# Kernel optimization log

Hardware: AMD Instinct MI355X
Metric: run time of the kernel (lower is better)

The kernel has to match this reference:

```python
import jax, jax.numpy as jnp
import numpy as np

HEAD_DIM = 64
NUM_FEATURES = 256


def _sample_orf(head_dim, num_features, seed=0):
    """Orthogonal random features with chi(d)-norm row scaling (FAVOR+)."""
    rng = np.random.RandomState(seed)
    blocks = []
    while len(blocks) * head_dim < num_features:
        G = rng.randn(head_dim, head_dim).astype(np.float32)
        Q, _ = np.linalg.qr(G)
        norms = np.linalg.norm(rng.randn(head_dim, head_dim).astype(np.float32), axis=1)
        blocks.append(np.diag(norms) @ Q.T)
    return np.concatenate(blocks, axis=0)[:num_features].astype(np.float32)


def _phi(x, omega, is_query):
    """FAVOR+ positive feature map with max-subtraction stabilization."""
    m = omega.shape[0]
    proj = jnp.einsum('bhnd,md->bhnm', x, omega)          # [B,H,N,M]
    norm = 0.5 * jnp.sum(x * x, axis=-1, keepdims=True)    # [B,H,N,1]
    log_phi = proj - norm
    if is_query:
        log_phi = log_phi - jnp.max(log_phi, axis=-1, keepdims=True)
    else:
        log_phi = log_phi - jnp.max(log_phi)
    return jnp.exp(log_phi) / np.float32(np.sqrt(m)) + 1e-4


def _causal_scan(phi_q, phi_k, v):
    """Causal linear-attention recurrence via lax.scan. States: S[B,H,M,D], z[B,H,M]."""
    B, H, N, M = phi_q.shape
    D = v.shape[-1]
    # seq-first for scan: [N,B,H,*]
    pq = jnp.moveaxis(phi_q, 2, 0)
    pk = jnp.moveaxis(phi_k, 2, 0)
    vt = jnp.moveaxis(v, 2, 0)

    S0 = jnp.zeros((B, H, M, D), dtype=phi_q.dtype)
    z0 = jnp.zeros((B, H, M), dtype=phi_q.dtype)

    def step(carry, xs):
        S, z = carry
        pq_i, pk_i, v_i = xs  # [B,H,M], [B,H,M], [B,H,D]
        S = S + pk_i[..., :, None] * v_i[..., None, :]
        z = z + pk_i
        num = jnp.einsum('bhm,bhmd->bhd', pq_i, S)
        den = jnp.sum(pq_i * z, axis=-1, keepdims=True) + 1e-6
        return (S, z), num / den

    _, out = jax.lax.scan(step, (S0, z0), (pq, pk, vt))  # out: [N,B,H,D]
    return jnp.moveaxis(out, 0, 2)


def setup_inputs() -> dict:
    key = jax.random.key(0)
    k1, k2, k3 = jax.random.split(key, 3)
    B, H, N, D = 2, 16, 4096, HEAD_DIM
    q = jax.random.normal(k1, (B, H, N, D), dtype=jnp.float32)
    k = jax.random.normal(k2, (B, H, N, D), dtype=jnp.float32)
    v = jax.random.normal(k3, (B, H, N, D), dtype=jnp.float32)
    omega = jnp.asarray(_sample_orf(HEAD_DIM, NUM_FEATURES))
    return {"q": q, "k": k, "v": v, "omega": omega}


def reference(q, k, v, omega):
    scale = q.shape[-1] ** (-0.25)
    phi_q = _phi(q * scale, omega, is_query=True)
    phi_k = _phi(k * scale, omega, is_query=False)
    # q_len == kv_len -> causal scan branch (matches original forward)
    out = _causal_scan(phi_q.astype(jnp.float32), phi_k.astype(jnp.float32),
                       v.astype(jnp.float32))
    return out.astype(q.dtype)
```

## Files before the change

kernel.cpp:

```cpp
#include <hip/hip_runtime.h>
#include <cstddef>

#define BH    32
#define NSEQ  4096
#define MFEAT 256
#define CHUNK 128
#define NCH   32
#define SROW  65
#define SPITCH (SROW*256)

#define SCALE 0.35355339059327373f

typedef unsigned int uint_t;
typedef _Float16 half_t;
typedef __attribute__((ext_vector_type(8))) _Float16 half8;
typedef __attribute__((ext_vector_type(4))) float f32x4;

__device__ __forceinline__ f32x4 mfma16(half8 a, half8 b, f32x4 c) {
  return __builtin_amdgcn_mfma_f32_16x16x32_f16(a, b, c, 0, 0, 0);
}
__device__ __forceinline__ uint_t enc_f(float x) {
  uint_t u = __float_as_uint(x);
  return (u & 0x80000000u) ? ~u : (u | 0x80000000u);
}
__device__ __forceinline__ float dec_f(uint_t u) {
  u = (u & 0x80000000u) ? (u ^ 0x80000000u) : ~u;
  return __uint_as_float(u);
}
__device__ __forceinline__ half8 cvt_h8(float4 a, float4 b) {
  half8 h;
  h[0] = (half_t)a.x; h[1] = (half_t)a.y; h[2] = (half_t)a.z; h[3] = (half_t)a.w;
  h[4] = (half_t)b.x; h[5] = (half_t)b.y; h[6] = (half_t)b.z; h[7] = (half_t)b.w;
  return h;
}

__global__ void k_init(uint_t* kmax) { *kmax = enc_f(-__builtin_inff()); }

__global__ __launch_bounds__(256, 4) void k_maxes(
    const float* __restrict__ q, const float* __restrict__ kx,
    const float* __restrict__ omega, float* __restrict__ rowmQ,
    uint_t* __restrict__ kmax)
{
  __shared__ half_t Wl[256 * 72];
  __shared__ float nrm[64];
  __shared__ float red[4];

  const int tid = threadIdx.x;
  const int lane = tid & 63;
  const int w = tid >> 6;
  const int lc = lane & 15, rg = lane >> 4, koff = rg * 8;
  const size_t rowbase = (size_t)blockIdx.x * 64;

  for (int l = tid; l < 4096; l += 256) {
    int m = l >> 4, d4 = (l & 15) * 4;
    float4 o = *(const float4*)(omega + m * 64 + d4);
    half_t* p = &Wl[m * 72 + d4];
    p[0] = (half_t)o.x; p[1] = (half_t)o.y; p[2] = (half_t)o.z; p[3] = (half_t)o.w;
  }
  half8 aq[2], akf[2];
  {
    const float* qp = q + (rowbase + w * 16 + lc) * 64 + koff;
    const float* kp = kx + (rowbase + w * 16 + lc) * 64 + koff;
    float pn = 0.f;
    #pragma unroll
    for (int ks = 0; ks < 2; ks++) {
      float4 a = *(const float4*)(qp + ks * 32);
      float4 b = *(const float4*)(qp + ks * 32 + 4);
      a.x *= SCALE; a.y *= SCALE; a.z *= SCALE; a.w *= SCALE;
      b.x *= SCALE; b.y *= SCALE; b.z *= SCALE; b.w *= SCALE;
      aq[ks] = cvt_h8(a, b);
      float4 c = *(const float4*)(kp + ks * 32);
      float4 d = *(const float4*)(kp + ks * 32 + 4);
      c.x *= SCALE; c.y *= SCALE; c.z *= SCALE; c.w *= SCALE;
      d.x *= SCALE; d.y *= SCALE; d.z *= SCALE; d.w *= SCALE;
      pn += c.x * c.x + c.y * c.y + c.z * c.z + c.w * c.w
          + d.x * d.x + d.y * d.y + d.z * d.z + d.w * d.w;
      akf[ks] = cvt_h8(c, d);
    }
    pn += __shfl_xor(pn, 16, 64);
    pn += __shfl_xor(pn, 32, 64);
    if (rg == 0) nrm[w * 16 + lc] = 0.5f * pn;
  }
  __syncthreads();

  float mrow[4] = {-3.4e38f, -3.4e38f, -3.4e38f, -3.4e38f};
  #pragma unroll
  for (int hh = 0; hh < 2; hh++) {
    f32x4 acc[8];
    #pragma unroll
    for (int c = 0; c < 8; c++) acc[c] = (f32x4){0.f, 0.f, 0.f, 0.f};
    #pragma unroll
    for (int ks = 0; ks < 2; ks++)
      #pragma unroll
      for (int c = 0; c < 8; c++) {
        half8 b = *(const half8*)&Wl[((hh * 8 + c) * 16 + lc) * 72 + ks * 32 + koff];
        acc[c] = mfma16(aq[ks], b, acc[c]);
      }
    #pragma unroll
    for (int c = 0; c < 8; c++)
      #pragma unroll
      for (int r = 0; r < 4; r++) mrow[r] = fmaxf(mrow[r], acc[c][r]);
  }
  #pragma unroll
  for (int r = 0; r < 4; r++) {
    float m0 = mrow[r];
    m0 = fmaxf(m0, __shfl_xor(m0, 1, 64));
    m0 = fmaxf(m0, __shfl_xor(m0, 2, 64));
    m0 = fmaxf(m0, __shfl_xor(m0, 4, 64));
    m0 = fmaxf(m0, __shfl_xor(m0, 8, 64));
    if (lc == 0) rowmQ[rowbase + w * 16 + rg * 4 + r] = m0;
  }

  float hn[4];
  #pragma unroll
  for (int r = 0; r < 4; r++) hn[r] = nrm[w * 16 + rg * 4 + r];
  float bm = -3.4e38f;
  #pragma unroll
  for (int hh = 0; hh < 2; hh++) {
    f32x4 acc[8];
    #pragma unroll
    for (int c = 0; c < 8; c++) acc[c] = (f32x4){0.f, 0.f, 0.f, 0.f};
    #pragma unroll
    for (int ks = 0; ks < 2; ks++)
      #pragma unroll
      for (int c = 0; c < 8; c++) {
        half8 b = *(const half8*)&Wl[((hh * 8 + c) * 16 + lc) * 72 + ks * 32 + koff];
        acc[c] = mfma16(akf[ks], b, acc[c]);
      }
    #pragma unroll
    for (int c = 0; c < 8; c++)
      #pragma unroll
      for (int r = 0; r < 4; r++) bm = fmaxf(bm, acc[c][r] - hn[r]);
  }
  #pragma unroll
  for (int off = 1; off < 64; off <<= 1) bm = fmaxf(bm, __shfl_xor(bm, off, 64));
  if (lane == 0) red[w] = bm;
  __syncthreads();
  if (tid == 0)
    atomicMax(kmax, enc_f(fmaxf(fmaxf(red[0], red[1]), fmaxf(red[2], red[3]))));
}

__global__ __launch_bounds__(256, 2) void k_state(
    const float* __restrict__ kx, const float* __restrict__ v,
    const float* __restrict__ omega, const uint_t* __restrict__ kmax,
    half_t* __restrict__ spA)
{
  __shared__ half_t WP[256 * 72];
  __shared__ half_t vt[80 * 136];
  __shared__ float nrmK[128];

  const int tid = threadIdx.x;
  const int lane = tid & 63;
  const int w = tid >> 6;
  const int lc = lane & 15, rg = lane >> 4, koff = rg * 8;
  const int wr = w * 32;
  const int blk = blockIdx.x;
  const size_t nbase = (size_t)(blk >> 5) * NSEQ + (size_t)(blk & 31) * CHUNK;
  const float gmaxv = dec_f(*kmax);

  for (int l = tid; l < 4096; l += 256) {
    int m = l >> 4, d4 = (l & 15) * 4;
    float4 o = *(const float4*)(omega + m * 64 + d4);
    half_t* p = &WP[m * 72 + d4];
    p[0] = (half_t)o.x; p[1] = (half_t)o.y; p[2] = (half_t)o.z; p[3] = (half_t)o.w;
  }
  for (int l = tid; l < 2048; l += 256) {
    int j = l >> 4, dq = (l & 15) * 4;
    float4 vv = *(const float4*)(v + (nbase + j) * 64 + dq);
    vt[(dq + 0) * 136 + j] = (half_t)vv.x;
    vt[(dq + 1) * 136 + j] = (half_t)vv.y;
    vt[(dq + 2) * 136 + j] = (half_t)vv.z;
    vt[(dq + 3) * 136 + j] = (half_t)vv.w;
  }
  if (tid < 128) vt[64 * 136 + tid] = (half_t)1.0f;

  half8 ak[2][2];
  float pn[2] = {0.f, 0.f};
  #pragma unroll
  for (int rt = 0; rt < 2; rt++) {
    const float* kp = kx + (nbase + wr + rt * 16 + lc) * 64 + koff;
    #pragma unroll
    for (int ks = 0; ks < 2; ks++) {
      float4 a = *(const float4*)(kp + ks * 32);
      float4 b = *(const float4*)(kp + ks * 32 + 4);
      a.x *= SCALE; a.y *= SCALE; a.z *= SCALE; a.w *= SCALE;
      b.x *= SCALE; b.y *= SCALE; b.z *= SCALE; b.w *= SCALE;
      pn[rt] += a.x * a.x + a.y * a.y + a.z * a.z + a.w * a.w
              + b.x * b.x + b.y * b.y + b.z * b.z + b.w * b.w;
      ak[rt][ks] = cvt_h8(a, b);
    }
    pn[rt] += __shfl_xor(pn[rt], 16, 64);
    pn[rt] += __shfl_xor(pn[rt], 32, 64);
  }
  if (rg == 0) {
    nrmK[wr + lc] = 0.5f * pn[0];
    nrmK[wr + 16 + lc] = 0.5f * pn[1];
  }
  __syncthreads();

  f32x4 accP[2][16];
  #pragma unroll
  for (int rt = 0; rt < 2; rt++)
    #pragma unroll
    for (int ct = 0; ct < 16; ct++) accP[rt][ct] = (f32x4){0.f, 0.f, 0.f, 0.f};
  #pragma unroll
  for (int ks = 0; ks < 2; ks++)
    #pragma unroll
    for (int ct = 0; ct < 16; ct++) {
      half8 b = *(const half8*)&WP[(ct * 16 + lc) * 72 + ks * 32 + koff];
      accP[0][ct] = mfma16(ak[0][ks], b, accP[0][ct]);
      accP[1][ct] = mfma16(ak[1][ks], b, accP[1][ct]);
    }
  float hnr[2][4];
  #pragma unroll
  for (int rt = 0; rt < 2; rt++)
    #pragma unroll
    for (int r = 0; r < 4; r++) hnr[rt][r] = nrmK[wr + rt * 16 + rg * 4 + r];
  #pragma unroll
  for (int rt = 0; rt < 2; rt++)
    #pragma unroll
    for (int ct = 0; ct < 16; ct++)
      #pragma unroll
      for (int r = 0; r < 4; r++)
        accP[rt][ct][r] = __expf(accP[rt][ct][r] - hnr[rt][r] - gmaxv) * 0.0625f + 1e-4f;

  half_t* pkT = WP;
  #pragma unroll
  for (int h = 0; h < 2; h++) {
    __syncthreads();
    #pragma unroll
    for (int rt = 0; rt < 2; rt++)
      #pragma unroll
      for (int c8 = 0; c8 < 8; c8++) {
        int ct = h * 8 + c8;
        #pragma unroll
        for (int r = 0; r < 4; r++)
          pkT[(c8 * 16 + lc) * 144 + wr + rt * 16 + rg * 4 + r] = (half_t)accP[rt][ct][r];
      }
    __syncthreads();
    f32x4 acc2[5][2];
    #pragma unroll
    for (int rt = 0; rt < 5; rt++) {
      acc2[rt][0] = (f32x4){0.f, 0.f, 0.f, 0.f};
      acc2[rt][1] = (f32x4){0.f, 0.f, 0.f, 0.f};
    }
    #pragma unroll
    for (int ks = 0; ks < 4; ks++) {
      half8 b0 = *(const half8*)&pkT[((2 * w + 0) * 16 + lc) * 144 + ks * 32 + koff];
      half8 b1 = *(const half8*)&pkT[((2 * w + 1) * 16 + lc) * 144 + ks * 32 + koff];
      #pragma unroll
      for (int rt = 0; rt < 5; rt++) {
        half8 a = *(const half8*)&vt[(rt * 16 + lc) * 136 + ks * 32 + koff];
        acc2[rt][0] = mfma16(a, b0, acc2[rt][0]);
        acc2[rt][1] = mfma16(a, b1, acc2[rt][1]);
      }
    }
    #pragma unroll
    for (int rt = 0; rt < 5; rt++)
      #pragma unroll
      for (int c2 = 0; c2 < 2; c2++)
        #pragma unroll
        for (int r = 0; r < 4; r++) {
          int row = rt * 16 + rg * 4 + r;
          if (row < SROW)
            spA[(size_t)blk * SPITCH + row * 256 + h * 128 + (2 * w + c2) * 16 + lc] =
                (half_t)acc2[rt][c2][r];
        }
  }
}

__global__ __launch_bounds__(256) void k_prefix(
    const uint_t* __restrict__ spA, uint_t* __restrict__ spB)
{
  int r = blockIdx.x * 256 + threadIdx.x;
  if (r >= SPITCH / 2) return;
  int bh = blockIdx.y;
  const uint_t* src = spA + (size_t)bh * NCH * (SPITCH / 2) + r;
  uint_t* dst = spB + (size_t)bh * NCH * (SPITCH / 2) + r;
  float r0 = 0.f, r1 = 0.f;
  for (int c = 0; c < NCH; c++) {
    union { uint_t u; half_t h[2]; } cv, ov;
    cv.u = src[(size_t)c * (SPITCH / 2)];
    ov.h[0] = (half_t)r0; ov.h[1] = (half_t)r1;
    dst[(size_t)c * (SPITCH / 2)] = ov.u;
    r0 += (float)cv.h[0];
    r1 += (float)cv.h[1];
  }
}

__global__ __launch_bounds__(256, 2) void k_attn4(
    const float* __restrict__ q, const float* __restrict__ kx,
    const float* __restrict__ v, const float* __restrict__ omega,
    const float* __restrict__ rowmQ, const uint_t* __restrict__ kmax,
    const half_t* __restrict__ spB, float* __restrict__ out)
{
  __shared__ half_t sm[37888];
  __shared__ float nrmK[128];
  half_t* Wl  = sm;
  half_t* PQ  = sm + 16384;
  half_t* PK  = sm + 24576;
  half_t* SST = sm + 32768;
  half_t* AS  = sm + 16384;
  half_t* VT  = sm + 24576;

  const int tid = threadIdx.x;
  const int lane = tid & 63;
  const int w = tid >> 6;
  const int lc = lane & 15, rg = lane >> 4, koff = rg * 8;
  const int wr = w * 32;
  const int blk = blockIdx.x;
  const size_t nbase = (size_t)(blk >> 5) * NSEQ + (size_t)(blk & 31) * CHUNK;
  const half_t* spb = spB + (size_t)blk * SPITCH;
  const float gmaxv = dec_f(*kmax);
  const int swz = (lc & 7) << 3;

  for (int l = tid; l < 2048; l += 256) {
    int m = l >> 3, d8 = (l & 7) * 8;
    float4 a = *(const float4*)(omega + m * 64 + d8);
    float4 b = *(const float4*)(omega + m * 64 + d8 + 4);
    *(half8*)&Wl[m * 64 + (d8 ^ ((m & 7) << 3))] = cvt_h8(a, b);
  }
  for (int l = tid; l < 480; l += 256)
    ((uint_t*)&SST[65 * 64])[l] = 0u;

  float rowm[2][4];
  #pragma unroll
  for (int rt = 0; rt < 2; rt++)
    #pragma unroll
    for (int r = 0; r < 4; r++)
      rowm[rt][r] = rowmQ[nbase + wr + rt * 16 + rg * 4 + r];

  half8 aq[2][2], ak[2][2];
  float pn[2] = {0.f, 0.f};
  #pragma unroll
  for (int rt = 0; rt < 2; rt++) {
    const float* qp = q + (nbase + wr + rt * 16 + lc) * 64 + koff;
    const float* kp = kx + (nbase + wr + rt * 16 + lc) * 64 + koff;
    #pragma unroll
    for (int ks = 0; ks < 2; ks++) {
      float4 a = *(const float4*)(qp + ks * 32);
      float4 b = *(const float4*)(qp + ks * 32 + 4);
      a.x *= SCALE; a.y *= SCALE; a.z *= SCALE; a.w *= SCALE;
      b.x *= SCALE; b.y *= SCALE; b.z *= SCALE; b.w *= SCALE;
      aq[rt][ks] = cvt_h8(a, b);
      float4 c = *(const float4*)(kp + ks * 32);
      float4 d = *(const float4*)(kp + ks * 32 + 4);
      c.x *= SCALE; c.y *= SCALE; c.z *= SCALE; c.w *= SCALE;
      d.x *= SCALE; d.y *= SCALE; d.z *= SCALE; d.w *= SCALE;
      pn[rt] += c.x * c.x + c.y * c.y + c.z * c.z + c.w * c.w
              + d.x * d.x + d.y * d.y + d.z * d.z + d.w * d.w;
      ak[rt][ks] = cvt_h8(c, d);
    }
    pn[rt] += __shfl_xor(pn[rt], 16, 64);
    pn[rt] += __shfl_xor(pn[rt], 32, 64);
  }
  if (rg == 0) {
    nrmK[wr + lc] = 0.5f * pn[0];
    nrmK[wr + 16 + lc] = 0.5f * pn[1];
  }

  half8 sstA, sstB, sstC = half8{};

#define LOADSST(MT) do {                                                      \
    { int l = tid;       int ro = l >> 3, c8 = (l & 7) * 8;                   \
      sstA = *(const half8*)(spb + ro * 256 + (MT) * 64 + c8); }              \
    { int l = tid + 256; int ro = l >> 3, c8 = (l & 7) * 8;                   \
      sstB = *(const half8*)(spb + ro * 256 + (MT) * 64 + c8); }              \
    if (tid < 8) { int l = tid + 512; int ro = l >> 3, c8 = (l & 7) * 8;      \
      sstC = *(const half8*)(spb + ro * 256 + (MT) * 64 + c8); }              \
  } while (0)

#define STAGEPHASE(MT) do {                                                   \
    { int l = tid;       int ro = l >> 3, c8 = (l & 7) * 8;                   \
      *(half8*)&SST[ro * 64 + (c8 ^ ((ro & 7) << 3))] = sstA; }               \
    { int l = tid + 256; int ro = l >> 3, c8 = (l & 7) * 8;                   \
      *(half8*)&SST[ro * 64 + (c8 ^ ((ro & 7) << 3))] = sstB; }               \
    if (tid < 8) { int l = tid + 512; int ro = l >> 3, c8 = (l & 7) * 8;      \
      *(half8*)&SST[ro * 64 + (c8 ^ ((ro & 7) << 3))] = sstC; }               \
    half8 bwl[4][2];                                                          \
    _Pragma("unroll") for (int ct = 0; ct < 4; ct++)                          \
      _Pragma("unroll") for (int ks = 0; ks < 2; ks++)                        \
        bwl[ct][ks] = *(const half8*)&Wl[((MT) * 64 + ct * 16 + lc) * 64      \
                                         + ((ks * 32 + koff) ^ swz)];         \
    f32x4 accP[2][4];                                                         \
    _Pragma("unroll") for (int rt = 0; rt < 2; rt++)                          \
      _Pragma("unroll") for (int ct = 0; ct < 4; ct++)                        \
        accP[rt][ct] = (f32x4){0.f, 0.f, 0.f, 0.f};                           \
    _Pragma("unroll") for (int ks = 0; ks < 2; ks++)                          \
      _Pragma("unroll") for (int ct = 0; ct < 4; ct++) {                      \
        accP[0][ct] = mfma16(aq[0][ks], bwl[ct][ks], accP[0][ct]);            \
        accP[1][ct] = mfma16(aq[1][ks], bwl[ct][ks], accP[1][ct]);            \
      }                                                                       \
    _Pragma("unroll") for (int rt = 0; rt < 2; rt++)                          \
      _Pragma("unroll") for (int ct = 0; ct < 4; ct++)                        \
        _Pragma("unroll") for (int r = 0; r < 4; r++) {                       \
          int i = wr + rt * 16 + rg * 4 + r;                                  \
          float val = __expf(accP[rt][ct][r] - rowm[rt][r]) * 0.0625f + 1e-4f;\
          PQ[i * 64 + ((ct * 16 + lc) ^ ((i & 7) << 3))] = (half_t)val;       \
        }                                                                     \
    _Pragma("unroll") for (int rt = 0; rt < 2; rt++)                          \
      _Pragma("unroll") for (int ct = 0; ct < 4; ct++)                        \
        accP[rt][ct] = (f32x4){0.f, 0.f, 0.f, 0.f};                           \
    _Pragma("unroll") for (int ks = 0; ks < 2; ks++)                          \
      _Pragma("unroll") for (int ct = 0; ct < 4; ct++) {                      \
        accP[0][ct] = mfma16(ak[0][ks], bwl[ct][ks], accP[0][ct]);            \
        accP[1][ct] = mfma16(ak[1][ks], bwl[ct][ks], accP[1][ct]);            \
      }                                                                       \
    _Pragma("unroll") for (int rt = 0; rt < 2; rt++)                          \
      _Pragma("unroll") for (int ct = 0; ct < 4; ct++)                        \
        _Pragma("unroll") for (int r = 0; r < 4; r++) {                       \
          int i = wr + rt * 16 + rg * 4 + r;                                  \
          float val = __expf(accP[rt][ct][r] - hnr[rt][r] - gmaxv) * 0.0625f + 1e-4f; \
          PK[i * 64 + ((ct * 16 + lc) ^ ((i & 7) << 3))] = (half_t)val;       \
        }                                                                     \
  } while (0)

#define COMPUTEPHASE() do {                                                   \
    _Pragma("unroll") for (int ks2 = 0; ks2 < 64; ks2 += 32) {                \
      int sA = (ks2 + koff) ^ swz;                                            \
      half8 a0 = *(const half8*)&PQ[(wr + lc) * 64 + sA];                     \
      half8 a1 = *(const half8*)&PQ[(wr + 16 + lc) * 64 + sA];                \
      _Pragma("unroll") for (int ct = 0; ct < 8; ct++) {                      \
        half8 b = *(const half8*)&PK[(ct * 16 + lc) * 64 + sA];               \
        accA[0][ct] = mfma16(a0, b, accA[0][ct]);                             \
        accA[1][ct] = mfma16(a1, b, accA[1][ct]);                             \
      }                                                                       \
      _Pragma("unroll") for (int cs = 0; cs < 5; cs++) {                      \
        half8 b = *(const half8*)&SST[(cs * 16 + lc) * 64 + sA];              \
        accO[0][cs] = mfma16(a0, b, accO[0][cs]);                             \
        accO[1][cs] = mfma16(a1, b, accO[1][cs]);                             \
      }                                                                       \
    } } while (0)

  LOADSST(0);
  __syncthreads();
  float hnr[2][4];
  #pragma unroll
  for (int rt = 0; rt < 2; rt++)
    #pragma unroll
    for (int r = 0; r < 4; r++) hnr[rt][r] = nrmK[wr + rt * 16 + rg * 4 + r];

  f32x4 accA[2][8], accO[2][5];
  #pragma unroll
  for (int rt = 0; rt < 2; rt++) {
    #pragma unroll
    for (int ct = 0; ct < 8; ct++) accA[rt][ct] = (f32x4){0.f, 0.f, 0.f, 0.f};
    #pragma unroll
    for (int cs = 0; cs < 5; cs++) accO[rt][cs] = (f32x4){0.f, 0.f, 0.f, 0.f};
  }

  float4 vv0, vv1, vv2, vv3, vv4, vv5, vv6, vv7;

  STAGEPHASE(0);
  __syncthreads();
  LOADSST(1);
  COMPUTEPHASE();
  __syncthreads();
  STAGEPHASE(1);
  __syncthreads();
  LOADSST(2);
  COMPUTEPHASE();
  __syncthreads();
  STAGEPHASE(2);
  __syncthreads();
  LOADSST(3);
  COMPUTEPHASE();
  __syncthreads();
  STAGEPHASE(3);
  __syncthreads();
  {
    const float* vb = v + nbase * 64;
    vv0 = *(const float4*)(vb + ((tid + 0 * 256) >> 4) * 64 + ((tid + 0 * 256) & 15) * 4);
    vv1 = *(const float4*)(vb + ((tid + 1 * 256) >> 4) * 64 + ((tid + 1 * 256) & 15) * 4);
    vv2 = *(const float4*)(vb + ((tid + 2 * 256) >> 4) * 64 + ((tid + 2 * 256) & 15) * 4);
    vv3 = *(const float4*)(vb + ((tid + 3 * 256) >> 4) * 64 + ((tid + 3 * 256) & 15) * 4);
    vv4 = *(const float4*)(vb + ((tid + 4 * 256) >> 4) * 64 + ((tid + 4 * 256) & 15) * 4);
    vv5 = *(const float4*)(vb + ((tid + 5 * 256) >> 4) * 64 + ((tid + 5 * 256) & 15) * 4);
    vv6 = *(const float4*)(vb + ((tid + 6 * 256) >> 4) * 64 + ((tid + 6 * 256) & 15) * 4);
    vv7 = *(const float4*)(vb + ((tid + 7 * 256) >> 4) * 64 + ((tid + 7 * 256) & 15) * 4);
  }
  COMPUTEPHASE();
  __syncthreads();

#define PUTV(VV, E) do {                                                      \
    int l = tid + (E) * 256; int j = l >> 4, dq = (l & 15) * 4;               \
    VT[(dq + 0) * 128 + (j ^ (((dq + 0) & 7) << 3))] = (half_t)VV.x;          \
    VT[(dq + 1) * 128 + (j ^ (((dq + 1) & 7) << 3))] = (half_t)VV.y;          \
    VT[(dq + 2) * 128 + (j ^ (((dq + 2) & 7) << 3))] = (half_t)VV.z;          \
    VT[(dq + 3) * 128 + (j ^ (((dq + 3) & 7) << 3))] = (half_t)VV.w;          \
  } while (0)
  PUTV(vv0, 0); PUTV(vv1, 1); PUTV(vv2, 2); PUTV(vv3, 3);
  PUTV(vv4, 4); PUTV(vv5, 5); PUTV(vv6, 6); PUTV(vv7, 7);
  if (tid < 128) VT[64 * 128 + tid] = (half_t)1.0f;

  #pragma unroll
  for (int h = 0; h < 2; h++) {
    #pragma unroll
    for (int rt = 0; rt < 2; rt++)
      #pragma unroll
      for (int c4 = 0; c4 < 4; c4++) {
        int ct = h * 4 + c4;
        int j = ct * 16 + lc;
        #pragma unroll
        for (int r = 0; r < 4; r++) {
          int i = wr + rt * 16 + rg * 4 + r;
          float val = (j <= i) ? accA[rt][ct][r] : 0.f;
          AS[i * 64 + ((j - h * 64) ^ ((i & 7) << 3))] = (half_t)val;
        }
      }
    if (h == 0) __syncthreads();
    #pragma unroll
    for (int ks2 = 0; ks2 < 64; ks2 += 32) {
      int sA = (ks2 + koff) ^ swz;
      int sV = (h * 64 + ks2 + koff) ^ swz;
      half8 a0 = *(const half8*)&AS[(wr + lc) * 64 + sA];
      half8 a1 = *(const half8*)&AS[(wr + 16 + lc) * 64 + sA];
      #pragma unroll
      for (int cs = 0; cs < 5; cs++) {
        half8 b = *(const half8*)&VT[(cs * 16 + lc) * 128 + sV];
        accO[0][cs] = mfma16(a0, b, accO[0][cs]);
        accO[1][cs] = mfma16(a1, b, accO[1][cs]);
      }
    }
  }

  __syncthreads();
  float* OS = (float*)sm;
  #pragma unroll
  for (int rt = 0; rt < 2; rt++)
    #pragma unroll
    for (int r = 0; r < 4; r++) {
      float den = __shfl(accO[rt][4][r], (lane & 48), 64) + 1e-6f;
      float inv = 1.0f / den;
      int i = wr + rt * 16 + rg * 4 + r;
      #pragma unroll
      for (int cs = 0; cs < 4; cs++)
        OS[i * 68 + cs * 16 + lc] = accO[rt][cs][r] * inv;
    }
  __syncthreads();
  #pragma unroll
  for (int e = 0; e < 8; e++) {
    int l = tid + e * 256;
    int row = l >> 4, c4 = (l & 15) * 4;
    float4 t4 = *(const float4*)&OS[row * 68 + c4];
    *(float4*)(out + (nbase + row) * 64 + c4) = t4;
  }
#undef LOADSST
#undef STAGEPHASE
#undef COMPUTEPHASE
#undef PUTV
}

extern "C" void kernel_launch(void* const* d_in, const int* in_sizes, int n_in,
                              void* d_out, int out_size, void* d_ws, size_t ws_size,
                              hipStream_t stream) {
  const float* q = (const float*)d_in[0];
  const float* k = (const float*)d_in[1];
  const float* v = (const float*)d_in[2];
  const float* omega = (const float*)d_in[3];
  float* out = (float*)d_out;
  char* ws = (char*)d_ws;

  float*  rowmQ = (float*)(ws + 0);
  half_t* spA   = (half_t*)(ws + 524288);
  half_t* spB   = (half_t*)(ws + 34603008);
  uint_t* kmax  = (uint_t*)(ws + 68681728);

  k_init<<<1, 1, 0, stream>>>(kmax);
  k_maxes<<<2048, 256, 0, stream>>>(q, k, omega, rowmQ, kmax);
  k_state<<<1024, 256, 0, stream>>>(k, v, omega, kmax, spA);
  k_prefix<<<dim3(33, 32), 256, 0, stream>>>((const uint_t*)spA, (uint_t*)spB);
  k_attn4<<<1024, 256, 0, stream>>>(q, k, v, omega, rowmQ, kmax, spB, out);
}
```

Before: 151.6 us.

## Cache scaled fp16 Q/K and key norms in workspace for downstream kernels

The max-finding kernel now writes the scaled fp16 Q and K tiles and the per-row key half-norms to workspace. The state and attention kernels read these directly instead of reloading fp32 Q/K, rescaling, converting and recomputing norms. The attention kernel also drops its LDS copy of omega and loads omega fragments from global memory per tile, which shrinks shared memory and removes a barrier. The cost is extra global writes in the first kernel and repeated uncached-looking omega loads in the inner staging phase.

```diff
diff --git a/kernel.cpp b/kernel.cpp
--- a/kernel.cpp
+++ b/kernel.cpp
@@ -36,10 +36,11 @@
 
 __global__ void k_init(uint_t* kmax) { *kmax = enc_f(-__builtin_inff()); }
 
-__global__ __launch_bounds__(256, 4) void k_maxes(
+__global__ __launch_bounds__(256, 4) void k_maxes2(
     const float* __restrict__ q, const float* __restrict__ kx,
     const float* __restrict__ omega, float* __restrict__ rowmQ,
-    uint_t* __restrict__ kmax)
+    uint_t* __restrict__ kmax, half_t* __restrict__ qh,
+    half_t* __restrict__ kh, float* __restrict__ hnKg)
 {
   __shared__ half_t Wl[256 * 72];
   __shared__ float nrm[64];
@@ -77,9 +78,17 @@
           + d.x * d.x + d.y * d.y + d.z * d.z + d.w * d.w;
       akf[ks] = cvt_h8(c, d);
     }
+    #pragma unroll
+    for (int ks = 0; ks < 2; ks++) {
+      *(half8*)(qh + (rowbase + w * 16 + lc) * 64 + ks * 32 + koff) = aq[ks];
+      *(half8*)(kh + (rowbase + w * 16 + lc) * 64 + ks * 32 + koff) = akf[ks];
+    }
     pn += __shfl_xor(pn, 16, 64);
     pn += __shfl_xor(pn, 32, 64);
-    if (rg == 0) nrm[w * 16 + lc] = 0.5f * pn;
+    if (rg == 0) {
+      nrm[w * 16 + lc] = 0.5f * pn;
+      hnKg[rowbase + w * 16 + lc] = 0.5f * pn;
+    }
   }
   __syncthreads();
 
@@ -140,14 +149,13 @@
     atomicMax(kmax, enc_f(fmaxf(fmaxf(red[0], red[1]), fmaxf(red[2], red[3]))));
 }
 
-__global__ __launch_bounds__(256, 2) void k_state(
-    const float* __restrict__ kx, const float* __restrict__ v,
-    const float* __restrict__ omega, const uint_t* __restrict__ kmax,
-    half_t* __restrict__ spA)
+__global__ __launch_bounds__(256, 2) void k_state2(
+    const half_t* __restrict__ kh, const float* __restrict__ v,
+    const float* __restrict__ omega, const float* __restrict__ hnKg,
+    const uint_t* __restrict__ kmax, half_t* __restrict__ spA)
 {
   __shared__ half_t WP[256 * 72];
   __shared__ half_t vt[80 * 136];
-  __shared__ float nrmK[128];
 
   const int tid = threadIdx.x;
   const int lane = tid & 63;
@@ -175,26 +183,15 @@
   if (tid < 128) vt[64 * 136 + tid] = (half_t)1.0f;
 
   half8 ak[2][2];
-  float pn[2] = {0.f, 0.f};
+  float hnr[2][4];
   #pragma unroll
   for (int rt = 0; rt < 2; rt++) {
-    const float* kp = kx + (nbase + wr + rt * 16 + lc) * 64 + koff;
-    #pragma unroll
-    for (int ks = 0; ks < 2; ks++) {
-      float4 a = *(const float4*)(kp + ks * 32);
-      float4 b = *(const float4*)(kp + ks * 32 + 4);
-      a.x *= SCALE; a.y *= SCALE; a.z *= SCALE; a.w *= SCALE;
-      b.x *= SCALE; b.y *= SCALE; b.z *= SCALE; b.w *= SCALE;
-      pn[rt] += a.x * a.x + a.y * a.y + a.z * a.z + a.w * a.w
-              + b.x * b.x + b.y * b.y + b.z * b.z + b.w * b.w;
-      ak[rt][ks] = cvt_h8(a, b);
-    }
-    pn[rt] += __shfl_xor(pn[rt], 16, 64);
-    pn[rt] += __shfl_xor(pn[rt], 32, 64);
-  }
-  if (rg == 0) {
-    nrmK[wr + lc] = 0.5f * pn[0];
-    nrmK[wr + 16 + lc] = 0.5f * pn[1];
+    const half_t* kp = kh + (nbase + wr + rt * 16 + lc) * 64 + koff;
+    ak[rt][0] = *(const half8*)(kp);
+    ak[rt][1] = *(const half8*)(kp + 32);
+    #pragma unroll
+    for (int r = 0; r < 4; r++)
+      hnr[rt][r] = hnKg[nbase + wr + rt * 16 + rg * 4 + r];
   }
   __syncthreads();
 
@@ -211,11 +208,6 @@
       accP[0][ct] = mfma16(ak[0][ks], b, accP[0][ct]);
       accP[1][ct] = mfma16(ak[1][ks], b, accP[1][ct]);
     }
-  float hnr[2][4];
-  #pragma unroll
-  for (int rt = 0; rt < 2; rt++)
-    #pragma unroll
-    for (int r = 0; r < 4; r++) hnr[rt][r] = nrmK[wr + rt * 16 + rg * 4 + r];
   #pragma unroll
   for (int rt = 0; rt < 2; rt++)
     #pragma unroll
@@ -288,20 +280,19 @@
   }
 }
 
-__global__ __launch_bounds__(256, 2) void k_attn4(
-    const float* __restrict__ q, const float* __restrict__ kx,
+__global__ __launch_bounds__(256, 2) void k_attn6(
+    const half_t* __restrict__ qh, const half_t* __restrict__ kh,
     const float* __restrict__ v, const float* __restrict__ omega,
-    const float* __restrict__ rowmQ, const uint_t* __restrict__ kmax,
-    const half_t* __restrict__ spB, float* __restrict__ out)
+    const float* __restrict__ rowmQ, const float* __restrict__ hnKg,
+    const uint_t* __restrict__ kmax, const half_t* __restrict__ spB,
+    float* __restrict__ out)
 {
-  __shared__ half_t sm[37888];
-  __shared__ float nrmK[128];
-  half_t* Wl  = sm;
-  half_t* PQ  = sm + 16384;
-  half_t* PK  = sm + 24576;
-  half_t* SST = sm + 32768;
-  half_t* AS  = sm + 16384;
-  half_t* VT  = sm + 24576;
+  __shared__ half_t sm[21504];
+  half_t* PQ  = sm;
+  half_t* PK  = sm + 8192;
+  half_t* SST = sm + 16384;
+  half_t* AS  = sm;
+  half_t* VT  = sm + 8192;
 
   const int tid = threadIdx.x;
   const int lane = tid & 63;
@@ -314,49 +305,23 @@
   const float gmaxv = dec_f(*kmax);
   const int swz = (lc & 7) << 3;
 
-  for (int l = tid; l < 2048; l += 256) {
-    int m = l >> 3, d8 = (l & 7) * 8;
-    float4 a = *(const float4*)(omega + m * 64 + d8);
-    float4 b = *(const float4*)(omega + m * 64 + d8 + 4);
-    *(half8*)&Wl[m * 64 + (d8 ^ ((m & 7) << 3))] = cvt_h8(a, b);
-  }
-  for (int l = tid; l < 480; l += 256)
-    ((uint_t*)&SST[65 * 64])[l] = 0u;
-
-  float rowm[2][4];
+  float rowm[2][4], hnr[2][4];
   #pragma unroll
   for (int rt = 0; rt < 2; rt++)
     #pragma unroll
-    for (int r = 0; r < 4; r++)
+    for (int r = 0; r < 4; r++) {
       rowm[rt][r] = rowmQ[nbase + wr + rt * 16 + rg * 4 + r];
-
+      hnr[rt][r]  = hnKg[nbase + wr + rt * 16 + rg * 4 + r];
+    }
   half8 aq[2][2], ak[2][2];
-  float pn[2] = {0.f, 0.f};
   #pragma unroll
   for (int rt = 0; rt < 2; rt++) {
-    const float* qp = q + (nbase + wr + rt * 16 + lc) * 64 + koff;
-    const float* kp = kx + (nbase + wr + rt * 16 + lc) * 64 + koff;
-    #pragma unroll
-    for (int ks = 0; ks < 2; ks++) {
-      float4 a = *(const float4*)(qp + ks * 32);
-      float4 b = *(const float4*)(qp + ks * 32 + 4);
-      a.x *= SCALE; a.y *= SCALE; a.z *= SCALE; a.w *= SCALE;
-      b.x *= SCALE; b.y *= SCALE; b.z *= SCALE; b.w *= SCALE;
-      aq[rt][ks] = cvt_h8(a, b);
-      float4 c = *(const float4*)(kp + ks * 32);
-      float4 d = *(const float4*)(kp + ks * 32 + 4);
-      c.x *= SCALE; c.y *= SCALE; c.z *= SCALE; c.w *= SCALE;
-      d.x *= SCALE; d.y *= SCALE; d.z *= SCALE; d.w *= SCALE;
-      pn[rt] += c.x * c.x + c.y * c.y + c.z * c.z + c.w * c.w
-              + d.x * d.x + d.y * d.y + d.z * d.z + d.w * d.w;
-      ak[rt][ks] = cvt_h8(c, d);
-    }
-    pn[rt] += __shfl_xor(pn[rt], 16, 64);
-    pn[rt] += __shfl_xor(pn[rt], 32, 64);
-  }
-  if (rg == 0) {
-    nrmK[wr + lc] = 0.5f * pn[0];
-    nrmK[wr + 16 + lc] = 0.5f * pn[1];
+    const half_t* qp = qh + (nbase + wr + rt * 16 + lc) * 64 + koff;
+    const half_t* kp = kh + (nbase + wr + rt * 16 + lc) * 64 + koff;
+    aq[rt][0] = *(const half8*)(qp);
+    aq[rt][1] = *(const half8*)(qp + 32);
+    ak[rt][0] = *(const half8*)(kp);
+    ak[rt][1] = *(const half8*)(kp + 32);
   }
 
   half8 sstA, sstB, sstC = half8{};
@@ -378,10 +343,12 @@
     if (tid < 8) { int l = tid + 512; int ro = l >> 3, c8 = (l & 7) * 8;      \
       *(half8*)&SST[ro * 64 + (c8 ^ ((ro & 7) << 3))] = sstC; }               \
     half8 bwl[4][2];                                                          \
-    _Pragma("unroll") for (int ct = 0; ct < 4; ct++)                          \
-      _Pragma("unroll") for (int ks = 0; ks < 2; ks++)                        \
-        bwl[ct][ks] = *(const half8*)&Wl[((MT) * 64 + ct * 16 + lc) * 64      \
-                                         + ((ks * 32 + koff) ^ swz)];         \
+    _Pragma("unroll") for (int ct = 0; ct < 4; ct++) {                        \
+      const float* op = omega + ((MT) * 64 + ct * 16 + lc) * 64 + koff;       \
+      bwl[ct][0] = cvt_h8(*(const float4*)(op), *(const float4*)(op + 4));    \
+      bwl[ct][1] = cvt_h8(*(const float4*)(op + 32),                          \
+                          *(const float4*)(op + 36));                         \
+    }                                                                         \
     f32x4 accP[2][4];                                                         \
     _Pragma("unroll") for (int rt = 0; rt < 2; rt++)                          \
       _Pragma("unroll") for (int ct = 0; ct < 4; ct++)                        \
@@ -433,12 +400,6 @@
     } } while (0)
 
   LOADSST(0);
-  __syncthreads();
-  float hnr[2][4];
-  #pragma unroll
-  for (int rt = 0; rt < 2; rt++)
-    #pragma unroll
-    for (int r = 0; r < 4; r++) hnr[rt][r] = nrmK[wr + rt * 16 + rg * 4 + r];
 
   f32x4 accA[2][8], accO[2][5];
   #pragma unroll
@@ -562,13 +523,16 @@
   char* ws = (char*)d_ws;
 
   float*  rowmQ = (float*)(ws + 0);
-  half_t* spA   = (half_t*)(ws + 524288);
-  half_t* spB   = (half_t*)(ws + 34603008);
-  uint_t* kmax  = (uint_t*)(ws + 68681728);
+  float*  hnKg  = (float*)(ws + 524288);
+  half_t* qh    = (half_t*)(ws + 1048576);
+  half_t* kh    = (half_t*)(ws + 17825792);
+  half_t* spA   = (half_t*)(ws + 34603008);
+  half_t* spB   = (half_t*)(ws + 68681728);
+  uint_t* kmax  = (uint_t*)(ws + 102760448);
 
   k_init<<<1, 1, 0, stream>>>(kmax);
-  k_maxes<<<2048, 256, 0, stream>>>(q, k, omega, rowmQ, kmax);
-  k_state<<<1024, 256, 0, stream>>>(k, v, omega, kmax, spA);
+  k_maxes2<<<2048, 256, 0, stream>>>(q, k, omega, rowmQ, kmax, qh, kh, hnKg);
+  k_state2<<<1024, 256, 0, stream>>>(kh, v, omega, hnKg, kmax, spA);
   k_prefix<<<dim3(33, 32), 256, 0, stream>>>((const uint_t*)spA, (uint_t*)spB);
-  k_attn4<<<1024, 256, 0, stream>>>(q, k, v, omega, rowmQ, kmax, spB, out);
-}
+  k_attn6<<<1024, 256, 0, stream>>>(qh, kh, v, omega, rowmQ, hnKg, kmax, spB, out);
+}
```

Measured after the change: 168.0 us. +10.9%, slower.
